# Performance work log

Hardware: AMD Instinct MI355X
Metric: run time of the kernel (lower is better)

Reference implementation:

```python
import jax, jax.numpy as jnp
import numpy as np

BETA = 0.25

def setup_inputs() -> dict:
    key = jax.random.key(0)
    k1, k2 = jax.random.split(key)
    x = jax.random.normal(k1, (32, 32, 32, 64), dtype=jnp.float32)
    # tf.random_uniform_initializer default: uniform in [-0.05, 0.05]
    embeddings = jax.random.uniform(k2, (64, 1024), dtype=jnp.float32,
                                    minval=-0.05, maxval=0.05)
    return {"x": x, "embeddings": embeddings}

def reference(x, embeddings):
    D, K = embeddings.shape
    flat = x.reshape(-1, D)                                   # [N, D]
    # squared L2 distances to each codebook vector (expanded form)
    sim = flat @ embeddings                                   # [N, K]
    dists = (jnp.sum(flat * flat, axis=1, keepdims=True)
             + jnp.sum(embeddings * embeddings, axis=0)
             - 2.0 * sim)                                     # [N, K]
    idx = jnp.argmin(dists, axis=1)                           # [N]
    quantized = embeddings.T[idx].reshape(x.shape)            # gather == one-hot matmul
    commitment_loss = BETA * jnp.mean((jax.lax.stop_gradient(quantized) - x) ** 2)
    codebook_loss = jnp.mean((quantized - jax.lax.stop_gradient(x)) ** 2)
    loss = commitment_loss + codebook_loss
    out = x + jax.lax.stop_gradient(quantized - x)            # straight-through
    return out, loss
```

## Files before the change

kernel.cpp:

```cpp
#include <hip/hip_runtime.h>
#include <hip/hip_bf16.h>


#define NROWS 32768
#define DDIM  64
#define KCODE 1024
#define NELEM (NROWS * DDIM)
#define MARGIN 2.5e-4f
#define FIXBLOCKS 256

typedef __attribute__((ext_vector_type(8))) short bf16x8;
typedef __attribute__((ext_vector_type(4))) float f32x4;

static __device__ __forceinline__ unsigned short f2bf(float v) {
    __hip_bfloat16 h = __float2bfloat16(v);
    unsigned short b;
    __builtin_memcpy(&b, &h, 2);
    return b;
}
static __device__ __forceinline__ float bf2f(unsigned short b) {
    unsigned int u = ((unsigned int)b) << 16;
    float f;
    __builtin_memcpy(&f, &u, 4);
    return f;
}

__global__ void vq_prep(const float* __restrict__ e,
                        float* __restrict__ se,
                        float* __restrict__ eT,
                        unsigned short* __restrict__ ehT,
                        unsigned short* __restrict__ elT,
                        int* __restrict__ ctrl) {
    __shared__ float tile[64][17];
    const int t = threadIdx.x;
    const int k0 = blockIdx.x * 16;
    if (blockIdx.x == 0 && t < 4) ctrl[t] = 0;
    #pragma unroll
    for (int i = 0; i < 4; ++i) {
        int idx = i * 256 + t;
        int d = idx >> 4, kk = idx & 15;
        tile[d][kk] = e[d * KCODE + k0 + kk];
    }
    __syncthreads();
    if (t < 16) {
        float s = 0.f;
        #pragma unroll
        for (int d = 0; d < 64; ++d) { float v = tile[d][t]; s = fmaf(v, v, s); }
        se[k0 + t] = s;
    }
    const int kk = t >> 4;
    const int dg = (t & 15) * 4;
    float v0 = tile[dg + 0][kk], v1 = tile[dg + 1][kk];
    float v2 = tile[dg + 2][kk], v3 = tile[dg + 3][kk];
    *(float4*)&eT[(size_t)(k0 + kk) * 64 + dg] = make_float4(v0, v1, v2, v3);
    unsigned short h0 = f2bf(v0), h1 = f2bf(v1), h2 = f2bf(v2), h3 = f2bf(v3);
    *(ushort4*)&ehT[(size_t)(k0 + kk) * 64 + dg] = make_ushort4(h0, h1, h2, h3);
    *(ushort4*)&elT[(size_t)(k0 + kk) * 64 + dg] =
        make_ushort4(f2bf(v0 - bf2f(h0)), f2bf(v1 - bf2f(h1)),
                     f2bf(v2 - bf2f(h2)), f2bf(v3 - bf2f(h3)));
}

__launch_bounds__(256, 2)
__global__ void vq_main(const float* __restrict__ x,
                        const float* __restrict__ se,
                        const float* __restrict__ eT,
                        const unsigned short* __restrict__ ehT,
                        const unsigned short* __restrict__ elT,
                        float* __restrict__ out,
                        float* __restrict__ lossAcc,
                        int* __restrict__ cnt,
                        int2* __restrict__ list) {
    __shared__ float Lb [64][65];
    __shared__ float Lb2[64][65];
    __shared__ int   Li [64][65];
    __shared__ int   rowIdx[64];
    __shared__ float wsum[4];

    const int t = threadIdx.x;
    const int lane = t & 63;
    const int w = t >> 6;
    const int quad = lane >> 4, l15 = lane & 15;
    const int rowBlk = blockIdx.x * 64;

    bf16x8 ah[4][2], al[4][2];
    #pragma unroll
    for (int mt = 0; mt < 4; ++mt) {
        #pragma unroll
        for (int ks = 0; ks < 2; ++ks) {
            const float4* ap = (const float4*)(x + (size_t)(rowBlk + mt * 16 + l15) * 64
                                               + ks * 32 + quad * 8);
            float4 a0 = ap[0], a1 = ap[1];
            float av[8] = {a0.x, a0.y, a0.z, a0.w, a1.x, a1.y, a1.z, a1.w};
            bf16x8 h, l;
            #pragma unroll
            for (int j = 0; j < 8; ++j) {
                unsigned short hb = f2bf(av[j]);
                h[j] = (short)hb;
                l[j] = (short)f2bf(av[j] - bf2f(hb));
            }
            ah[mt][ks] = h; al[mt][ks] = l;
        }
    }

    float sb[4][4], sb2[4][4];
    int   si[4][4];
    #pragma unroll
    for (int mt = 0; mt < 4; ++mt)
        #pragma unroll
        for (int r = 0; r < 4; ++r) { sb[mt][r] = 3.4e38f; sb2[mt][r] = 3.4e38f; si[mt][r] = 0; }

    const int cbase = w * 256;
    const size_t bStr = (size_t)64;
    bf16x8 h0[4], h1[4], l0[4], l1[4];
    float sen[4];
    #pragma unroll
    for (int p = 0; p < 4; ++p) {
        const int nl = cbase + p * 16 + l15;
        const bf16x8* hp = (const bf16x8*)(ehT + (size_t)nl * bStr + quad * 8);
        const bf16x8* lp = (const bf16x8*)(elT + (size_t)nl * bStr + quad * 8);
        h0[p] = hp[0]; h1[p] = hp[4]; l0[p] = lp[0]; l1[p] = lp[4];
        sen[p] = se[nl];
    }

    #pragma unroll 4
    for (int nt = 0; nt < 16; ++nt) {
        const int p = nt & 3;
        bf16x8 ch0 = h0[p], ch1 = h1[p], cl0 = l0[p], cl1 = l1[p];
        float cse = sen[p];
        {
            const int nl = cbase + (nt + 4) * 16 + l15;
            const bf16x8* hp = (const bf16x8*)(ehT + (size_t)nl * bStr + quad * 8);
            const bf16x8* lp = (const bf16x8*)(elT + (size_t)nl * bStr + quad * 8);
            h0[p] = hp[0]; h1[p] = hp[4]; l0[p] = lp[0]; l1[p] = lp[4];
            sen[p] = se[nl];
        }
        const int nl = cbase + nt * 16 + l15;
        #pragma unroll
        for (int mt = 0; mt < 4; ++mt) {
            f32x4 aA = {0.f, 0.f, 0.f, 0.f}, aB = {0.f, 0.f, 0.f, 0.f};
            aA = __builtin_amdgcn_mfma_f32_16x16x32_bf16(ah[mt][0], ch0, aA, 0, 0, 0);
            aB = __builtin_amdgcn_mfma_f32_16x16x32_bf16(ah[mt][1], ch1, aB, 0, 0, 0);
            aA = __builtin_amdgcn_mfma_f32_16x16x32_bf16(ah[mt][0], cl0, aA, 0, 0, 0);
            aB = __builtin_amdgcn_mfma_f32_16x16x32_bf16(ah[mt][1], cl1, aB, 0, 0, 0);
            aA = __builtin_amdgcn_mfma_f32_16x16x32_bf16(al[mt][0], ch0, aA, 0, 0, 0);
            aB = __builtin_amdgcn_mfma_f32_16x16x32_bf16(al[mt][1], ch1, aB, 0, 0, 0);
            #pragma unroll
            for (int r = 0; r < 4; ++r) {
                float key = fmaf(-2.f, aA[r] + aB[r], cse);
                bool lt = key < sb[mt][r];
                sb2[mt][r] = fminf(sb2[mt][r], fmaxf(sb[mt][r], key));
                sb[mt][r]  = fminf(sb[mt][r], key);
                si[mt][r]  = lt ? nl : si[mt][r];
            }
        }
    }

    const int col = w * 16 + l15;
    #pragma unroll
    for (int mt = 0; mt < 4; ++mt)
        #pragma unroll
        for (int r = 0; r < 4; ++r) {
            int rr = mt * 16 + quad * 4 + r;
            Lb [rr][col] = sb [mt][r];
            Lb2[rr][col] = sb2[mt][r];
            Li [rr][col] = si [mt][r];
        }
    __syncthreads();

    if (t < 64) {
        float B = Lb[t][0], B2 = Lb2[t][0];
        int I = Li[t][0];
        for (int c = 1; c < 64; ++c) {
            float b = Lb[t][c], b2 = Lb2[t][c];
            int i = Li[t][c];
            float nB2 = fminf(fminf(B2, b2), fmaxf(B, b));
            bool take = (b < B) || (b == B && i < I);
            B = take ? b : B;
            I = take ? i : I;
            B2 = nB2;
        }
        rowIdx[t] = I;
        if (B2 - B < MARGIN) {
            int p = atomicAdd(cnt, 1);
            list[p] = make_int2(rowBlk + t, I);
        }
    }
    __syncthreads();

    {
        const int rl = w * 16 + l15;
        const int idx = rowIdx[rl];
        const float4* qrow = (const float4*)(eT + (size_t)idx * 64 + quad * 16);
        const float4* xrow = (const float4*)(x + (size_t)(rowBlk + rl) * 64 + quad * 16);
        float4* orow = (float4*)(out + (size_t)(rowBlk + rl) * 64 + quad * 16);
        float lsum = 0.f;
        #pragma unroll
        for (int i = 0; i < 4; ++i) {
            float4 q = qrow[i];
            float4 xv = xrow[i];
            float4 o;
            float dx;
            dx = q.x - xv.x; o.x = xv.x + dx; lsum = fmaf(dx, dx, lsum);
            dx = q.y - xv.y; o.y = xv.y + dx; lsum = fmaf(dx, dx, lsum);
            dx = q.z - xv.z; o.z = xv.z + dx; lsum = fmaf(dx, dx, lsum);
            dx = q.w - xv.w; o.w = xv.w + dx; lsum = fmaf(dx, dx, lsum);
            orow[i] = o;
        }
        #pragma unroll
        for (int off = 32; off > 0; off >>= 1)
            lsum += __shfl_down(lsum, off, 64);
        if (lane == 0) wsum[w] = lsum;
    }
    __syncthreads();
    if (t == 0)
        atomicAdd(lossAcc, wsum[0] + wsum[1] + wsum[2] + wsum[3]);
}

__launch_bounds__(256)
__global__ void vq_fix(const float* __restrict__ x,
                       const float* __restrict__ se,
                       const float* __restrict__ eT,
                       const int2* __restrict__ list,
                       const int* __restrict__ cnt,
                       float* __restrict__ lossAcc,
                       int* __restrict__ done,
                       float* __restrict__ out) {
    __shared__ float xs[64];
    __shared__ float cb[256];
    __shared__ int   ci[256];
    __shared__ int   newIdxS;
    const int t = threadIdx.x;
    const int n = *cnt;

    for (int i = blockIdx.x; i < n; i += gridDim.x) {
        int2 en = list[i];
        const int row = en.x, oldIdx = en.y;
        if (t < 64) xs[t] = x[(size_t)row * 64 + t];
        __syncthreads();

        float sx = 0.f;
        #pragma unroll
        for (int d = 0; d < 64; ++d) sx = fmaf(xs[d], xs[d], sx);

        const int k0 = t * 4;
        const float4* e0 = (const float4*)(eT + (size_t)(k0 + 0) * 64);
        const float4* e1 = (const float4*)(eT + (size_t)(k0 + 1) * 64);
        const float4* e2 = (const float4*)(eT + (size_t)(k0 + 2) * 64);
        const float4* e3 = (const float4*)(eT + (size_t)(k0 + 3) * 64);
        float dot0 = 0.f, dot1 = 0.f, dot2 = 0.f, dot3 = 0.f;
        #pragma unroll
        for (int i4 = 0; i4 < 16; ++i4) {
            float4 v0 = e0[i4], v1 = e1[i4], v2 = e2[i4], v3 = e3[i4];
            float xa = xs[4 * i4 + 0], xb = xs[4 * i4 + 1];
            float xc = xs[4 * i4 + 2], xd = xs[4 * i4 + 3];
            dot0 = fmaf(xa, v0.x, dot0); dot0 = fmaf(xb, v0.y, dot0);
            dot0 = fmaf(xc, v0.z, dot0); dot0 = fmaf(xd, v0.w, dot0);
            dot1 = fmaf(xa, v1.x, dot1); dot1 = fmaf(xb, v1.y, dot1);
            dot1 = fmaf(xc, v1.z, dot1); dot1 = fmaf(xd, v1.w, dot1);
            dot2 = fmaf(xa, v2.x, dot2); dot2 = fmaf(xb, v2.y, dot2);
            dot2 = fmaf(xc, v2.z, dot2); dot2 = fmaf(xd, v2.w, dot2);
            dot3 = fmaf(xa, v3.x, dot3); dot3 = fmaf(xb, v3.y, dot3);
            dot3 = fmaf(xc, v3.z, dot3); dot3 = fmaf(xd, v3.w, dot3);
        }
        float dd0 = (sx + se[k0 + 0]) - 2.0f * dot0;
        float dd1 = (sx + se[k0 + 1]) - 2.0f * dot1;
        float dd2 = (sx + se[k0 + 2]) - 2.0f * dot2;
        float dd3 = (sx + se[k0 + 3]) - 2.0f * dot3;
        float db = dd0; int di = k0;
        if (dd1 < db) { db = dd1; di = k0 + 1; }
        if (dd2 < db) { db = dd2; di = k0 + 2; }
        if (dd3 < db) { db = dd3; di = k0 + 3; }
        cb[t] = db; ci[t] = di;
        __syncthreads();

        if (t < 64) {
            float B = cb[t]; int I = ci[t];
            #pragma unroll
            for (int s = 64; s < 256; s += 64) {
                float b = cb[t + s]; int i2 = ci[t + s];
                bool take = (b < B) || (b == B && i2 < I);
                B = take ? b : B;
                I = take ? i2 : I;
            }
            #pragma unroll
            for (int m = 1; m < 64; m <<= 1) {
                float ob = __shfl_xor(B, m, 64);
                int   oi = __shfl_xor(I, m, 64);
                bool take = (ob < B) || (ob == B && oi < I);
                B = take ? ob : B;
                I = take ? oi : I;
            }
            if (t == 0) newIdxS = I;
        }
        __syncthreads();

        const int ni = newIdxS;
        if (ni != oldIdx) {
            if (t < 64) {
                float xv = xs[t];
                float qn = eT[(size_t)ni * 64 + t];
                float qo = eT[(size_t)oldIdx * 64 + t];
                float dn = qn - xv, dl = qo - xv;
                out[(size_t)row * 64 + t] = xv + dn;
                float delta = dn * dn - dl * dl;
                #pragma unroll
                for (int off = 32; off > 0; off >>= 1)
                    delta += __shfl_down(delta, off, 64);
                if (t == 0) atomicAdd(lossAcc, delta);
            }
        }
        __syncthreads();
    }

    if (t == 0) {
        __threadfence();
        int fin = atomicAdd(done, 1);
        if (fin == FIXBLOCKS - 1) {
            float s = atomicAdd(lossAcc, 0.0f);
            float m = s / (float)NELEM;
            out[NELEM] = 0.25f * m + m;
        }
    }
}

extern "C" void kernel_launch(void* const* d_in, const int* in_sizes, int n_in,
                              void* d_out, int out_size, void* d_ws, size_t ws_size,
                              hipStream_t stream) {
    const float* x = (const float*)d_in[0];
    const float* e = (const float*)d_in[1];
    float* out = (float*)d_out;
    float* ws  = (float*)d_ws;

    float* lossAcc      = ws;
    int*   cnt          = (int*)(ws + 1);
    int*   done         = (int*)(ws + 2);
    float* se           = ws + 64;
    float* eT           = ws + 1280;
    unsigned short* ehT = (unsigned short*)(ws + 66816);
    unsigned short* elT = (unsigned short*)(ws + 101632);
    int2*  list         = (int2*)(ws + 136448);

    vq_prep<<<64, 256, 0, stream>>>(e, se, eT, ehT, elT, (int*)ws);
    vq_main<<<NROWS / 64, 256, 0, stream>>>(x, se, eT, ehT, elT, out, lossAcc, cnt, list);
    vq_fix<<<FIXBLOCKS, 256, 0, stream>>>(x, se, eT, list, cnt, lossAcc, done, out);
}
```

Baseline: 112.4 us.

## Stage fp16 codebook in LDS per block and cut split-precision MFMAs

The main kernel now copies the whole fp16 codebook (XOR-swizzled) into shared memory with global_load_lds. Each of 8 waves handles 16 rows against all 1024 codes, so the cross-wave shared-memory argmin reduction becomes a wave shuffle reduction. The codebook is kept only as fp16 high parts, which reduces MFMAs per tile from 6 to 4, and the margin for exact refinement is raised to absorb the larger error. Loss partials go to a per-block array that the last fix block reduces, replacing the global atomic. The risks are more rows sent to the fix kernel, 128KB of LDS per block with one block per CU, and fp16 range limits.

```diff
diff --git a/kernel.cpp b/kernel.cpp
--- a/kernel.cpp
+++ b/kernel.cpp
@@ -6,30 +6,29 @@
 #define DDIM  64
 #define KCODE 1024
 #define NELEM (NROWS * DDIM)
-#define MARGIN 2.5e-4f
+#define MARGIN 4e-3f
 #define FIXBLOCKS 256
-
-typedef __attribute__((ext_vector_type(8))) short bf16x8;
+#define MAINBLK 256
+
+typedef __attribute__((ext_vector_type(8))) _Float16 f16x8;
 typedef __attribute__((ext_vector_type(4))) float f32x4;
 
-static __device__ __forceinline__ unsigned short f2bf(float v) {
-    __hip_bfloat16 h = __float2bfloat16(v);
+static __device__ __forceinline__ unsigned short f2h(float v) {
+    _Float16 h = (_Float16)v;
     unsigned short b;
     __builtin_memcpy(&b, &h, 2);
     return b;
 }
-static __device__ __forceinline__ float bf2f(unsigned short b) {
-    unsigned int u = ((unsigned int)b) << 16;
-    float f;
-    __builtin_memcpy(&f, &u, 4);
-    return f;
+static __device__ __forceinline__ void gload16(const void* g, void* l) {
+    __builtin_amdgcn_global_load_lds(
+        (const __attribute__((address_space(1))) void*)g,
+        (__attribute__((address_space(3))) void*)l, 16, 0, 0);
 }
 
 __global__ void vq_prep(const float* __restrict__ e,
                         float* __restrict__ se,
                         float* __restrict__ eT,
-                        unsigned short* __restrict__ ehT,
-                        unsigned short* __restrict__ elT,
+                        unsigned short* __restrict__ ehSw,
                         int* __restrict__ ctrl) {
     __shared__ float tile[64][17];
     const int t = threadIdx.x;
@@ -50,149 +49,131 @@
     }
     const int kk = t >> 4;
     const int dg = (t & 15) * 4;
+    const int kg = k0 + kk;
     float v0 = tile[dg + 0][kk], v1 = tile[dg + 1][kk];
     float v2 = tile[dg + 2][kk], v3 = tile[dg + 3][kk];
-    *(float4*)&eT[(size_t)(k0 + kk) * 64 + dg] = make_float4(v0, v1, v2, v3);
-    unsigned short h0 = f2bf(v0), h1 = f2bf(v1), h2 = f2bf(v2), h3 = f2bf(v3);
-    *(ushort4*)&ehT[(size_t)(k0 + kk) * 64 + dg] = make_ushort4(h0, h1, h2, h3);
-    *(ushort4*)&elT[(size_t)(k0 + kk) * 64 + dg] =
-        make_ushort4(f2bf(v0 - bf2f(h0)), f2bf(v1 - bf2f(h1)),
-                     f2bf(v2 - bf2f(h2)), f2bf(v3 - bf2f(h3)));
-}
-
-__launch_bounds__(256, 2)
+    *(float4*)&eT[(size_t)kg * 64 + dg] = make_float4(v0, v1, v2, v3);
+    const int sw = (((dg >> 3) ^ (kg & 7)) << 3) + (dg & 7);
+    *(ushort4*)&ehSw[(size_t)kg * 64 + sw] =
+        make_ushort4(f2h(v0), f2h(v1), f2h(v2), f2h(v3));
+}
+
+__launch_bounds__(512)
 __global__ void vq_main(const float* __restrict__ x,
                         const float* __restrict__ se,
                         const float* __restrict__ eT,
-                        const unsigned short* __restrict__ ehT,
-                        const unsigned short* __restrict__ elT,
+                        const unsigned short* __restrict__ ehSw,
                         float* __restrict__ out,
-                        float* __restrict__ lossAcc,
+                        float* __restrict__ parts,
                         int* __restrict__ cnt,
                         int2* __restrict__ list) {
-    __shared__ float Lb [64][65];
-    __shared__ float Lb2[64][65];
-    __shared__ int   Li [64][65];
-    __shared__ int   rowIdx[64];
-    __shared__ float wsum[4];
+    __shared__ unsigned short Beh[KCODE * 64];
+    __shared__ float sse[KCODE];
+    __shared__ float wsum[8];
 
     const int t = threadIdx.x;
     const int lane = t & 63;
     const int w = t >> 6;
     const int quad = lane >> 4, l15 = lane & 15;
-    const int rowBlk = blockIdx.x * 64;
-
-    bf16x8 ah[4][2], al[4][2];
+    const int rowBase = blockIdx.x * 128 + w * 16;
+
+    {
+        const unsigned char* g = (const unsigned char*)ehSw;
+        #pragma unroll
+        for (int r = 0; r < 16; ++r)
+            gload16(g + (size_t)(r * 512 + t) * 16, &Beh[(r * 512 + t) * 8]);
+        float2 s2 = ((const float2*)se)[t];
+        sse[2 * t + 0] = s2.x;
+        sse[2 * t + 1] = s2.y;
+    }
+
+    f16x8 ah0, ah1, al0, al1;
+    {
+        const float4* ap0 = (const float4*)(x + (size_t)(rowBase + l15) * 64 + quad * 8);
+        const float4* ap1 = (const float4*)(x + (size_t)(rowBase + l15) * 64 + 32 + quad * 8);
+        float4 a0 = ap0[0], a1 = ap0[1], b0 = ap1[0], b1 = ap1[1];
+        float av[8] = {a0.x, a0.y, a0.z, a0.w, a1.x, a1.y, a1.z, a1.w};
+        float bv[8] = {b0.x, b0.y, b0.z, b0.w, b1.x, b1.y, b1.z, b1.w};
+        f16x8 h0, h1, l0, l1;
+        #pragma unroll
+        for (int j = 0; j < 8; ++j) {
+            _Float16 ha = (_Float16)av[j];
+            _Float16 hb = (_Float16)bv[j];
+            h0[j] = ha;
+            h1[j] = hb;
+            l0[j] = (_Float16)(av[j] - (float)ha);
+            l1[j] = (_Float16)(bv[j] - (float)hb);
+        }
+        ah0 = h0; ah1 = h1; al0 = l0; al1 = l1;
+    }
+    __syncthreads();
+
+    float sb[4], sb2[4];
+    int   si[4];
     #pragma unroll
-    for (int mt = 0; mt < 4; ++mt) {
-        #pragma unroll
-        for (int ks = 0; ks < 2; ++ks) {
-            const float4* ap = (const float4*)(x + (size_t)(rowBlk + mt * 16 + l15) * 64
-                                               + ks * 32 + quad * 8);
-            float4 a0 = ap[0], a1 = ap[1];
-            float av[8] = {a0.x, a0.y, a0.z, a0.w, a1.x, a1.y, a1.z, a1.w};
-            bf16x8 h, l;
-            #pragma unroll
-            for (int j = 0; j < 8; ++j) {
-                unsigned short hb = f2bf(av[j]);
-                h[j] = (short)hb;
-                l[j] = (short)f2bf(av[j] - bf2f(hb));
-            }
-            ah[mt][ks] = h; al[mt][ks] = l;
-        }
-    }
-
-    float sb[4][4], sb2[4][4];
-    int   si[4][4];
+    for (int r = 0; r < 4; ++r) { sb[r] = 3.4e38f; sb2[r] = 3.4e38f; si[r] = 0; }
+
+    const int slot0 = ((quad ^ (l15 & 7)) << 3);
+    const int slot1 = (((quad + 4) ^ (l15 & 7)) << 3);
+
+    #pragma unroll 4
+    for (int nt = 0; nt < 64; ++nt) {
+        const int code = nt * 16 + l15;
+        f16x8 b0 = *(const f16x8*)&Beh[code * 64 + slot0];
+        f16x8 b1 = *(const f16x8*)&Beh[code * 64 + slot1];
+        float cse = sse[code];
+        f32x4 aA = {0.f, 0.f, 0.f, 0.f}, aB = {0.f, 0.f, 0.f, 0.f};
+        aA = __builtin_amdgcn_mfma_f32_16x16x32_f16(ah0, b0, aA, 0, 0, 0);
+        aB = __builtin_amdgcn_mfma_f32_16x16x32_f16(ah1, b1, aB, 0, 0, 0);
+        aA = __builtin_amdgcn_mfma_f32_16x16x32_f16(al0, b0, aA, 0, 0, 0);
+        aB = __builtin_amdgcn_mfma_f32_16x16x32_f16(al1, b1, aB, 0, 0, 0);
+        #pragma unroll
+        for (int r = 0; r < 4; ++r) {
+            float key = fmaf(-2.f, aA[r] + aB[r], cse);
+            bool lt = key < sb[r];
+            sb2[r] = fminf(sb2[r], fmaxf(sb[r], key));
+            sb[r]  = fminf(sb[r], key);
+            si[r]  = lt ? code : si[r];
+        }
+    }
+
     #pragma unroll
-    for (int mt = 0; mt < 4; ++mt)
-        #pragma unroll
-        for (int r = 0; r < 4; ++r) { sb[mt][r] = 3.4e38f; sb2[mt][r] = 3.4e38f; si[mt][r] = 0; }
-
-    const int cbase = w * 256;
-    const size_t bStr = (size_t)64;
-    bf16x8 h0[4], h1[4], l0[4], l1[4];
-    float sen[4];
-    #pragma unroll
-    for (int p = 0; p < 4; ++p) {
-        const int nl = cbase + p * 16 + l15;
-        const bf16x8* hp = (const bf16x8*)(ehT + (size_t)nl * bStr + quad * 8);
-        const bf16x8* lp = (const bf16x8*)(elT + (size_t)nl * bStr + quad * 8);
-        h0[p] = hp[0]; h1[p] = hp[4]; l0[p] = lp[0]; l1[p] = lp[4];
-        sen[p] = se[nl];
-    }
-
-    #pragma unroll 4
-    for (int nt = 0; nt < 16; ++nt) {
-        const int p = nt & 3;
-        bf16x8 ch0 = h0[p], ch1 = h1[p], cl0 = l0[p], cl1 = l1[p];
-        float cse = sen[p];
-        {
-            const int nl = cbase + (nt + 4) * 16 + l15;
-            const bf16x8* hp = (const bf16x8*)(ehT + (size_t)nl * bStr + quad * 8);
-            const bf16x8* lp = (const bf16x8*)(elT + (size_t)nl * bStr + quad * 8);
-            h0[p] = hp[0]; h1[p] = hp[4]; l0[p] = lp[0]; l1[p] = lp[4];
-            sen[p] = se[nl];
-        }
-        const int nl = cbase + nt * 16 + l15;
-        #pragma unroll
-        for (int mt = 0; mt < 4; ++mt) {
-            f32x4 aA = {0.f, 0.f, 0.f, 0.f}, aB = {0.f, 0.f, 0.f, 0.f};
-            aA = __builtin_amdgcn_mfma_f32_16x16x32_bf16(ah[mt][0], ch0, aA, 0, 0, 0);
-            aB = __builtin_amdgcn_mfma_f32_16x16x32_bf16(ah[mt][1], ch1, aB, 0, 0, 0);
-            aA = __builtin_amdgcn_mfma_f32_16x16x32_bf16(ah[mt][0], cl0, aA, 0, 0, 0);
-            aB = __builtin_amdgcn_mfma_f32_16x16x32_bf16(ah[mt][1], cl1, aB, 0, 0, 0);
-            aA = __builtin_amdgcn_mfma_f32_16x16x32_bf16(al[mt][0], ch0, aA, 0, 0, 0);
-            aB = __builtin_amdgcn_mfma_f32_16x16x32_bf16(al[mt][1], ch1, aB, 0, 0, 0);
-            #pragma unroll
-            for (int r = 0; r < 4; ++r) {
-                float key = fmaf(-2.f, aA[r] + aB[r], cse);
-                bool lt = key < sb[mt][r];
-                sb2[mt][r] = fminf(sb2[mt][r], fmaxf(sb[mt][r], key));
-                sb[mt][r]  = fminf(sb[mt][r], key);
-                si[mt][r]  = lt ? nl : si[mt][r];
-            }
-        }
-    }
-
-    const int col = w * 16 + l15;
-    #pragma unroll
-    for (int mt = 0; mt < 4; ++mt)
+    for (int m = 1; m < 16; m <<= 1) {
         #pragma unroll
         for (int r = 0; r < 4; ++r) {
-            int rr = mt * 16 + quad * 4 + r;
-            Lb [rr][col] = sb [mt][r];
-            Lb2[rr][col] = sb2[mt][r];
-            Li [rr][col] = si [mt][r];
-        }
-    __syncthreads();
-
-    if (t < 64) {
-        float B = Lb[t][0], B2 = Lb2[t][0];
-        int I = Li[t][0];
-        for (int c = 1; c < 64; ++c) {
-            float b = Lb[t][c], b2 = Lb2[t][c];
-            int i = Li[t][c];
-            float nB2 = fminf(fminf(B2, b2), fmaxf(B, b));
-            bool take = (b < B) || (b == B && i < I);
-            B = take ? b : B;
-            I = take ? i : I;
-            B2 = nB2;
-        }
-        rowIdx[t] = I;
-        if (B2 - B < MARGIN) {
-            int p = atomicAdd(cnt, 1);
-            list[p] = make_int2(rowBlk + t, I);
-        }
-    }
-    __syncthreads();
+            float ob  = __shfl_xor(sb[r],  m, 64);
+            float ob2 = __shfl_xor(sb2[r], m, 64);
+            int   oi  = __shfl_xor(si[r],  m, 64);
+            float nb2 = fminf(fminf(sb2[r], ob2), fmaxf(sb[r], ob));
+            bool take = (ob < sb[r]) || (ob == sb[r] && oi < si[r]);
+            sb[r] = take ? ob : sb[r];
+            si[r] = take ? oi : si[r];
+            sb2[r] = nb2;
+        }
+    }
+
+    if (l15 == 0) {
+        #pragma unroll
+        for (int r = 0; r < 4; ++r) {
+            if (sb2[r] - sb[r] < MARGIN) {
+                int p = atomicAdd(cnt, 1);
+                list[p] = make_int2(rowBase + quad * 4 + r, si[r]);
+            }
+        }
+    }
+
+    int src = (l15 >> 2) << 4;
+    int j0 = __shfl(si[0], src, 64);
+    int j1 = __shfl(si[1], src, 64);
+    int j2 = __shfl(si[2], src, 64);
+    int j3 = __shfl(si[3], src, 64);
+    int rsel = l15 & 3;
+    int myidx = rsel == 0 ? j0 : (rsel == 1 ? j1 : (rsel == 2 ? j2 : j3));
 
     {
-        const int rl = w * 16 + l15;
-        const int idx = rowIdx[rl];
-        const float4* qrow = (const float4*)(eT + (size_t)idx * 64 + quad * 16);
-        const float4* xrow = (const float4*)(x + (size_t)(rowBlk + rl) * 64 + quad * 16);
-        float4* orow = (float4*)(out + (size_t)(rowBlk + rl) * 64 + quad * 16);
+        const float4* qrow = (const float4*)(eT + (size_t)myidx * 64 + quad * 16);
+        const float4* xrow = (const float4*)(x + (size_t)(rowBase + l15) * 64 + quad * 16);
+        float4* orow = (float4*)(out + (size_t)(rowBase + l15) * 64 + quad * 16);
         float lsum = 0.f;
         #pragma unroll
         for (int i = 0; i < 4; ++i) {
@@ -212,8 +193,12 @@
         if (lane == 0) wsum[w] = lsum;
     }
     __syncthreads();
-    if (t == 0)
-        atomicAdd(lossAcc, wsum[0] + wsum[1] + wsum[2] + wsum[3]);
+    if (t == 0) {
+        float s = 0.f;
+        #pragma unroll
+        for (int i = 0; i < 8; ++i) s += wsum[i];
+        parts[blockIdx.x] = s;
+    }
 }
 
 __launch_bounds__(256)
@@ -222,6 +207,7 @@
                        const float* __restrict__ eT,
                        const int2* __restrict__ list,
                        const int* __restrict__ cnt,
+                       const float* __restrict__ parts,
                        float* __restrict__ lossAcc,
                        int* __restrict__ done,
                        float* __restrict__ out) {
@@ -229,6 +215,7 @@
     __shared__ float cb[256];
     __shared__ int   ci[256];
     __shared__ int   newIdxS;
+    __shared__ int   lastS;
     const int t = threadIdx.x;
     const int n = *cnt;
 
@@ -315,10 +302,22 @@
     if (t == 0) {
         __threadfence();
         int fin = atomicAdd(done, 1);
-        if (fin == FIXBLOCKS - 1) {
-            float s = atomicAdd(lossAcc, 0.0f);
-            float m = s / (float)NELEM;
-            out[NELEM] = 0.25f * m + m;
+        lastS = (fin == FIXBLOCKS - 1) ? 1 : 0;
+    }
+    __syncthreads();
+    if (lastS) {
+        cb[t] = parts[t];
+        __syncthreads();
+        if (t < 64) {
+            float v = cb[t] + cb[t + 64] + cb[t + 128] + cb[t + 192];
+            #pragma unroll
+            for (int off = 32; off > 0; off >>= 1)
+                v += __shfl_down(v, off, 64);
+            if (t == 0) {
+                float total = v + atomicAdd(lossAcc, 0.0f);
+                float m = total / (float)NELEM;
+                out[NELEM] = 0.25f * m + m;
+            }
         }
     }
 }
@@ -331,16 +330,16 @@
     float* out = (float*)d_out;
     float* ws  = (float*)d_ws;
 
-    float* lossAcc      = ws;
-    int*   cnt          = (int*)(ws + 1);
-    int*   done         = (int*)(ws + 2);
-    float* se           = ws + 64;
-    float* eT           = ws + 1280;
-    unsigned short* ehT = (unsigned short*)(ws + 66816);
-    unsigned short* elT = (unsigned short*)(ws + 101632);
-    int2*  list         = (int2*)(ws + 136448);
-
-    vq_prep<<<64, 256, 0, stream>>>(e, se, eT, ehT, elT, (int*)ws);
-    vq_main<<<NROWS / 64, 256, 0, stream>>>(x, se, eT, ehT, elT, out, lossAcc, cnt, list);
-    vq_fix<<<FIXBLOCKS, 256, 0, stream>>>(x, se, eT, list, cnt, lossAcc, done, out);
-}
+    float* lossAcc       = ws;
+    int*   cnt           = (int*)(ws + 1);
+    int*   done          = (int*)(ws + 2);
+    float* se            = ws + 64;
+    float* eT            = ws + 1280;
+    unsigned short* ehSw = (unsigned short*)(ws + 66816);
+    int2*  list          = (int2*)(ws + 99584);
+    float* parts         = ws + 165120;
+
+    vq_prep<<<64, 256, 0, stream>>>(e, se, eT, ehSw, (int*)ws);
+    vq_main<<<MAINBLK, 512, 0, stream>>>(x, se, eT, ehSw, out, parts, cnt, list);
+    vq_fix<<<FIXBLOCKS, 256, 0, stream>>>(x, se, eT, list, cnt, parts, lossAcc, done, out);
+}
```

New measurement: 107.7 us. -4.2%, faster.
